# Optimization experiments

Measured on AMD Instinct MI355X. Metric: run time of the kernel, lower is better.

The kernel has to match this reference:

```python
import jax, jax.numpy as jnp
import numpy as np

# Static dims (match init_kwargs / input_specs)
N, F, C, H, W = 1, 60, 31, 64, 64
DIM = 60          # embed dim == F
WS = 8            # window_size
NH = 6            # num_heads
HD = DIM // NH    # head dim = 10
SHIFT = WS // 2   # shift for odd blocks
NWIN_TOK = WS * WS
MLP_HID = 4 * DIM
EPS = 1e-5


def _rel_pos_index(ws):
    # standard Swin relative position index, computed once in numpy
    coords = np.stack(np.meshgrid(np.arange(ws), np.arange(ws), indexing='ij'))  # (2, ws, ws)
    coords = coords.reshape(2, -1)                                                # (2, ws*ws)
    rel = coords[:, :, None] - coords[:, None, :]                                 # (2, n, n)
    rel = rel.transpose(1, 2, 0)
    rel[..., 0] += ws - 1
    rel[..., 1] += ws - 1
    rel[..., 0] *= 2 * ws - 1
    return rel.sum(-1)                                                            # (n, n)

RPI = jnp.asarray(_rel_pos_index(WS))  # (64, 64) int


def _attn_mask(h, w, ws, shift):
    # mask for shifted-window attention: -100 where tokens come from different regions
    img = np.zeros((h, w))
    cnt = 0
    for hs in (slice(0, -ws), slice(-ws, -shift), slice(-shift, None)):
        for wsl in (slice(0, -ws), slice(-ws, -shift), slice(-shift, None)):
            img[hs, wsl] = cnt
            cnt += 1
    m = img.reshape(h // ws, ws, w // ws, ws).transpose(0, 2, 1, 3).reshape(-1, ws * ws)  # (nW, n)
    diff = m[:, None, :] - m[:, :, None]
    return jnp.asarray(np.where(diff != 0, -100.0, 0.0).astype(np.float32))               # (nW, n, n)

ATTN_MASK = _attn_mask(H, W, WS, SHIFT)


def _ln(x, g, b):
    mu = jnp.mean(x, axis=-1, keepdims=True)
    var = jnp.mean(jnp.square(x - mu), axis=-1, keepdims=True)
    return (x - mu) * jax.lax.rsqrt(var + EPS) * g + b


def _swin_block(x, shift, g1, b1, qkv_w, qkv_b, rpb, proj_w, proj_b,
                g2, b2, fc1_w, fc1_b, fc2_w, fc2_b):
    # x: (B, L=H*W, DIM)
    B = x.shape[0]
    shortcut = x
    h = _ln(x, g1, b1).reshape(B, H, W, DIM)
    if shift > 0:
        h = jnp.roll(h, (-shift, -shift), axis=(1, 2))
    # window partition -> (B*nW, n, DIM)
    win = h.reshape(B, H // WS, WS, W // WS, WS, DIM).transpose(0, 1, 3, 2, 4, 5)
    win = win.reshape(-1, NWIN_TOK, DIM)
    Bw = win.shape[0]
    # qkv projection (torch Linear: y = x @ W.T + b)
    qkv = win @ qkv_w.T + qkv_b                                   # (Bw, n, 3*DIM)
    qkv = qkv.reshape(Bw, NWIN_TOK, 3, NH, HD).transpose(2, 0, 3, 1, 4)
    q, k, v = qkv[0], qkv[1], qkv[2]                              # (Bw, NH, n, HD)
    scale = HD ** -0.5
    attn = jnp.einsum('bhnd,bhmd->bhnm', q * scale, k)            # (Bw, NH, n, n)
    bias = rpb[RPI.reshape(-1)].reshape(NWIN_TOK, NWIN_TOK, NH).transpose(2, 0, 1)
    attn = attn + bias[None]
    if shift > 0:
        nW = ATTN_MASK.shape[0]
        attn = attn.reshape(-1, nW, NH, NWIN_TOK, NWIN_TOK) + ATTN_MASK[None, :, None]
        attn = attn.reshape(-1, NH, NWIN_TOK, NWIN_TOK)
    attn = jax.nn.softmax(attn, axis=-1)
    out = jnp.einsum('bhnm,bhmd->bhnd', attn, v).transpose(0, 2, 1, 3).reshape(Bw, NWIN_TOK, DIM)
    out = out @ proj_w.T + proj_b
    # window reverse -> (B, H, W, DIM)
    out = out.reshape(B, H // WS, W // WS, WS, WS, DIM).transpose(0, 1, 3, 2, 4, 5)
    out = out.reshape(B, H, W, DIM)
    if shift > 0:
        out = jnp.roll(out, (shift, shift), axis=(1, 2))
    x = shortcut + out.reshape(B, H * W, DIM)
    # MLP with exact GELU (torch nn.GELU default)
    h2 = _ln(x, g2, b2)
    h2 = jax.nn.gelu(h2 @ fc1_w.T + fc1_b, approximate=False) @ fc2_w.T + fc2_b
    return x + h2


def setup_inputs() -> dict:
    key = jax.random.key(0)
    ks = jax.random.split(key, 16)
    s = 0.02
    inp = {
        'x': jax.random.normal(ks[0], (N, F, C, H, W), jnp.float32),
        'norm1_g': jnp.ones((2, DIM), jnp.float32),
        'norm1_b': jnp.zeros((2, DIM), jnp.float32),
        'qkv_w': jax.random.normal(ks[1], (2, 3 * DIM, DIM), jnp.float32) * s,
        'qkv_b': jnp.zeros((2, 3 * DIM), jnp.float32),
        'rpb': jax.random.normal(ks[2], (2, (2 * WS - 1) ** 2, NH), jnp.float32) * s,
        'proj_w': jax.random.normal(ks[3], (2, DIM, DIM), jnp.float32) * s,
        'proj_b': jnp.zeros((2, DIM), jnp.float32),
        'norm2_g': jnp.ones((2, DIM), jnp.float32),
        'norm2_b': jnp.zeros((2, DIM), jnp.float32),
        'fc1_w': jax.random.normal(ks[4], (2, MLP_HID, DIM), jnp.float32) * s,
        'fc1_b': jnp.zeros((2, MLP_HID), jnp.float32),
        'fc2_w': jax.random.normal(ks[5], (2, DIM, MLP_HID), jnp.float32) * s,
        'fc2_b': jnp.zeros((2, DIM), jnp.float32),
    }
    return inp


def reference(x, norm1_g, norm1_b, qkv_w, qkv_b, rpb, proj_w, proj_b,
              norm2_g, norm2_b, fc1_w, fc1_b, fc2_w, fc2_b):
    # (N, F, C, H, W) -> (N*C, F, H, W) -> patch embed (flatten) -> (B, L, DIM)
    out = jnp.transpose(x, (0, 2, 1, 3, 4)).reshape(N * C, F, H, W)
    out = out.reshape(N * C, F, H * W).transpose(0, 2, 1)  # (B, L, DIM)
    for i in range(2):
        shift = 0 if i % 2 == 0 else SHIFT
        out = _swin_block(out, shift,
                          norm1_g[i], norm1_b[i], qkv_w[i], qkv_b[i], rpb[i],
                          proj_w[i], proj_b[i], norm2_g[i], norm2_b[i],
                          fc1_w[i], fc1_b[i], fc2_w[i], fc2_b[i])
    # patch unembed -> (B, F, H, W) -> (N, C, F, H, W) -> transpose(1,2)
    out = out.transpose(0, 2, 1).reshape(N * C, F, H, W)
    out = out.reshape(N, C, F, H, W)
    return jnp.transpose(out, (0, 2, 1, 3, 4))
```

## Files before the change

kernel.cpp:

```cpp
#include <hip/hip_runtime.h>
#include <hip/hip_bf16.h>
#include <math.h>


#define NB 31
#define NTOK 4096
#define DIM 60
#define NTOT (NB*NTOK)
#define QK_SCALE 0.31622776601683794f
#define LOG2E 1.4426950408889634f
#define QK_SCALE_L2E 0.45622000587446957f

typedef __attribute__((ext_vector_type(8))) short bf16x8;
typedef __attribute__((ext_vector_type(4))) float f32x4;

__device__ __forceinline__ short f2b(float f){
    return __builtin_bit_cast(short, __float2bfloat16(f));
}
__device__ __forceinline__ float b2f(unsigned short u){
    union{unsigned u;float f;}v; v.u=((unsigned)u)<<16; return v.f;
}
__device__ __forceinline__ unsigned pk2(float a,float b){
    return (unsigned)(unsigned short)f2b(a) | ((unsigned)(unsigned short)f2b(b)<<16);
}
#define MFMA16(a,b,c) __builtin_amdgcn_mfma_f32_16x16x32_bf16(a,b,c,0,0,0)
#define EXP2RAW(x) __builtin_amdgcn_exp2f(x)

#define PK_QKV  0
#define PK_PROJ 13824
#define PK_W1   18432
#define PK_W2   35712
#define PK_STRIDE 52608

__global__ __launch_bounds__(256) void pack_w(
    const float* __restrict__ qkv_w, const float* __restrict__ proj_w,
    const float* __restrict__ fc1_w, const float* __restrict__ fc2_w,
    const float* __restrict__ rpb, short* __restrict__ pk, float* __restrict__ btab)
{
    const int L = blockIdx.x;
    short* o = pk + (size_t)L * PK_STRIDE;
    const float* qw = qkv_w + L * 10800;
    const float* pw = proj_w + L * 3600;
    const float* w1 = fc1_w + L * 14400;
    const float* w2 = fc2_w + L * 14400;
    const float* rp = rpb + L * 1350;
    const int t0 = blockIdx.y * 256 + threadIdx.x;
    const int STP = 256 * gridDim.y;

    for (int i = t0; i < 192 * 72; i += STP) {
        int row = i / 72, k = i - row * 72;
        int p = row / 96, rg = row - p * 96;
        short v = 0;
        if (rg < 90 && k < 60) {
            int which = rg / 30, idx = rg - which * 30;
            int h = p * 3 + idx / 10, e = idx - (idx / 10) * 10;
            float wv = qw[(which * 60 + h * 10 + e) * 60 + k];
            if (which == 0) wv *= QK_SCALE_L2E;
            v = f2b(wv);
        }
        o[PK_QKV + i] = v;
    }
    for (int i = t0; i < 64 * 72; i += STP) {
        int n = i / 72, k = i - n * 72;
        o[PK_PROJ + i] = (n < 60 && k < 60) ? f2b(pw[n * 60 + k]) : (short)0;
    }
    for (int i = t0; i < 240 * 72; i += STP) {
        int n = i / 72, k = i - n * 72;
        o[PK_W1 + i] = (k < 60) ? f2b(w1[n * 60 + k]) : (short)0;
    }
    for (int i = t0; i < 64 * 264; i += STP) {
        int n = i / 264, k = i - n * 264;
        o[PK_W2 + i] = (n < 60 && k < 240) ? f2b(w2[n * 240 + k]) : (short)0;
    }
    const int NTAB = (L == 0) ? 24576 : 4 * 24576;
    float* bo = btab + (size_t)L * 4 * 24576;
    for (int i = t0; i < NTAB; i += STP) {
        int c = i / 24576, rem = i - c * 24576;
        int h = rem >> 12, rem2 = rem & 4095;
        int ii = rem2 >> 6, j = rem2 & 63;
        int iy = ii >> 3, ix = ii & 7, jy = j >> 3, jx = j & 7;
        float v = rp[((iy - jy + 7) * 15 + (ix - jx + 7)) * 6 + h];
        int riy = (c & 2) ? (iy < 4 ? 1 : 2) : 0;
        int rix = (c & 1) ? (ix < 4 ? 1 : 2) : 0;
        int rjy = (c & 2) ? (jy < 4 ? 1 : 2) : 0;
        int rjx = (c & 1) ? (jx < 4 ? 1 : 2) : 0;
        if (riy != rjy || rix != rjx) v -= 100.f;
        bo[i] = v * LOG2E;
    }
}

template<int L>
__global__ __launch_bounds__(256, 5) void swin_layer(
    const void* __restrict__ xin_v, void* __restrict__ xout_v,
    const float* __restrict__ g1, const float* __restrict__ b1,
    const float* __restrict__ g2, const float* __restrict__ b2,
    const short* __restrict__ pk, const float* __restrict__ btab,
    const float* __restrict__ qkv_b, const float* __restrict__ proj_b,
    const float* __restrict__ fc1_b, const float* __restrict__ fc2_b)
{
    __shared__ __attribute__((aligned(16))) short R1[64 * 72];
    __shared__ __attribute__((aligned(16))) short R2[8832];

    const f32x4 Z4 = {0.f, 0.f, 0.f, 0.f};
    const bf16x8 Z8 = {0, 0, 0, 0, 0, 0, 0, 0};

    const int tid = threadIdx.x;
    const int blk = ((blockIdx.x & 7) * 248) + (blockIdx.x >> 3);
    const int b = blk >> 6, w = blk & 63, wy = w >> 3, wx = w & 7;
    const int shift = L ? 4 : 0;
    const int cls = L ? (((wy == 7) ? 2 : 0) + ((wx == 7) ? 1 : 0)) : 0;

    const float* xf = (const float*)xin_v;
    const unsigned short* xb = (const unsigned short*)xin_v;

    for (int i = tid; i < 64 * 18; i += 256) {
        int row = i / 18, t = i - row * 18, bc = t / 3, k = t - bc * 3;
        *(int*)&R2[row * 104 + bc * 16 + 10 + 2 * k] = 0;
    }

    const int tk = tid >> 2, l4 = tid & 3;
    const int tok = (((wy * 8 + (tk >> 3) + shift) & 63) << 6)
                  + ((wx * 8 + (tk & 7) + shift) & 63);
    unsigned xpk[8];
    if (L == 0) {
        float xr[15]; float s = 0.f, s2 = 0.f;
#pragma unroll
        for (int dd = 0; dd < 15; ++dd) {
            float v = xf[(size_t)(l4 * 15 + dd) * NTOT + b * NTOK + tok];
            xr[dd] = v; s += v; s2 += v * v;
        }
        s  += __shfl_xor(s, 1);  s  += __shfl_xor(s, 2);
        s2 += __shfl_xor(s2, 1); s2 += __shfl_xor(s2, 2);
        const float mu = s * (1.f / 60.f);
        const float rs = rsqrtf(s2 * (1.f / 60.f) - mu * mu + 1e-5f);
#pragma unroll
        for (int dd = 0; dd < 15; ++dd) {
            int d = l4 * 15 + dd;
            R1[tk * 72 + d] = f2b((xr[dd] - mu) * rs * g1[d] + b1[d]);
        }
#pragma unroll
        for (int u = 0; u < 3; ++u) R1[tk * 72 + 60 + l4 * 3 + u] = 0;
#pragma unroll
        for (int u = 0; u < 7; ++u) xpk[u] = pk2(xr[2 * u], xr[2 * u + 1]);
        xpk[7] = pk2(xr[14], 0.f);
    } else {
        float xr[16]; float s = 0.f, s2 = 0.f;
        const int nd = (l4 == 3) ? 6 : 8, c0 = l4 * 16;
        const unsigned* rp_ = (const unsigned*)(xb + ((size_t)b * NTOK + tok) * DIM) + l4 * 8;
#pragma unroll
        for (int j = 0; j < 8; ++j) {
            if (j < nd) {
                unsigned u = rp_[j];
                xpk[j] = u;
                float v0 = b2f((unsigned short)(u & 0xffff));
                float v1 = b2f((unsigned short)(u >> 16));
                xr[2 * j] = v0; xr[2 * j + 1] = v1;
                s += v0 + v1; s2 += v0 * v0 + v1 * v1;
            }
        }
        s  += __shfl_xor(s, 1);  s  += __shfl_xor(s, 2);
        s2 += __shfl_xor(s2, 1); s2 += __shfl_xor(s2, 2);
        const float mu = s * (1.f / 60.f);
        const float rs = rsqrtf(s2 * (1.f / 60.f) - mu * mu + 1e-5f);
#pragma unroll
        for (int j = 0; j < 8; ++j) {
            if (j < nd) {
                int d = c0 + 2 * j;
                float n0 = (xr[2 * j] - mu) * rs * g1[d] + b1[d];
                float n1 = (xr[2 * j + 1] - mu) * rs * g1[d + 1] + b1[d + 1];
                *(unsigned*)&R1[tk * 72 + d] = pk2(n0, n1);
            }
        }
        if (l4 == 3) {
#pragma unroll
            for (int u = 0; u < 3; ++u) *(unsigned*)&R1[tk * 72 + 60 + 2 * u] = 0;
        }
    }

    const int lane = tid & 63, r16 = lane & 15, g = lane >> 4;
    const int m0 = (tid >> 6) << 4;

    bf16x8 a0 = *(const bf16x8*)&R1[(m0 + r16) * 72 + g * 8];
    bf16x8 a1 = *(const bf16x8*)&R1[(m0 + r16) * 72 + 32 + g * 8];
    const float* btc = btab + (size_t)cls * 24576 + (m0 + r16) * 64;

    for (int p = 0; p < 2; ++p) {
#pragma unroll
        for (int nt = 0; nt < 6; ++nt) {
            const short* wr = pk + PK_QKV + (size_t)(p * 96 + nt * 16 + r16) * 72;
            bf16x8 w0 = *(const bf16x8*)(wr + g * 8);
            bf16x8 w1v = *(const bf16x8*)(wr + 32 + g * 8);
            int c = nt * 16 + r16;
            int which = 0, hl = 0, e = 0; float bias = 0.f;
            if (c < 90) {
                which = c / 30; int idx = c - which * 30;
                hl = idx / 10; e = idx - hl * 10;
                bias = qkv_b[which * 60 + (p * 3 + hl) * 10 + e];
                if (which == 0) bias *= QK_SCALE_L2E;
            }
            f32x4 acc = {bias, bias, bias, bias};
            acc = MFMA16(a0, w0, acc);
            acc = MFMA16(a1, w1v, acc);
            if (c < 90) {
                if (which == 0) {
#pragma unroll
                    for (int r = 0; r < 4; ++r)
                        R2[(m0 + g * 4 + r) * 104 + hl * 16 + e] = f2b(acc[r]);
                } else if (which == 1) {
#pragma unroll
                    for (int r = 0; r < 4; ++r)
                        R2[(m0 + g * 4 + r) * 104 + 48 + hl * 16 + e] = f2b(acc[r]);
                } else {
#pragma unroll
                    for (int r = 0; r < 2; ++r)
                        *(unsigned*)&R2[6656 + (hl * 10 + e) * 72 + m0 + g * 4 + 2 * r] =
                            pk2(acc[2 * r], acc[2 * r + 1]);
                }
            }
        }
        __syncthreads();

#pragma unroll
        for (int hl = 0; hl < 3; ++hl) {
            const int h = p * 3 + hl;
            bf16x8 qa = Z8;
            if (g < 2) qa = *(const bf16x8*)&R2[(m0 + r16) * 104 + hl * 16 + g * 8];
            const float* bh = btc + h * 4096;
            f32x4 sv[4];
#pragma unroll
            for (int nt = 0; nt < 4; ++nt) {
                bf16x8 kb = Z8;
                if (g < 2) kb = *(const bf16x8*)&R2[(nt * 16 + r16) * 104 + 48 + hl * 16 + g * 8];
                sv[nt] = MFMA16(kb, qa, *(const f32x4*)&bh[nt * 16 + g * 4]);
            }
            float sum = 0.f;
#pragma unroll
            for (int nt = 0; nt < 4; ++nt)
#pragma unroll
                for (int r = 0; r < 4; ++r) {
                    float e = EXP2RAW(sv[nt][r]);
                    sv[nt][r] = e; sum += e;
                }
            sum += __shfl_xor(sum, 16);
            sum += __shfl_xor(sum, 32);
            const float inv = 1.f / sum;

            unsigned qd00 = pk2(sv[0][0], sv[0][1]), qd01 = pk2(sv[0][2], sv[0][3]);
            unsigned qd10 = pk2(sv[1][0], sv[1][1]), qd11 = pk2(sv[1][2], sv[1][3]);
            unsigned qd20 = pk2(sv[2][0], sv[2][1]), qd21 = pk2(sv[2][2], sv[2][3]);
            unsigned qd30 = pk2(sv[3][0], sv[3][1]), qd31 = pk2(sv[3][2], sv[3][3]);
            const int sA = (r16 + ((g & 1) << 5)) << 2;
            const int sB = sA + 64;
            const bool hi = (g >> 1) & 1;
            union { unsigned u[4]; bf16x8 v; } pb0, pb1;
            {
                unsigned x0 = __builtin_amdgcn_ds_bpermute(sA, (int)qd00);
                unsigned y0 = __builtin_amdgcn_ds_bpermute(sA, (int)qd10);
                pb0.u[0] = hi ? y0 : x0;
                unsigned x1 = __builtin_amdgcn_ds_bpermute(sA, (int)qd01);
                unsigned y1 = __builtin_amdgcn_ds_bpermute(sA, (int)qd11);
                pb0.u[1] = hi ? y1 : x1;
                unsigned x2 = __builtin_amdgcn_ds_bpermute(sB, (int)qd00);
                unsigned y2 = __builtin_amdgcn_ds_bpermute(sB, (int)qd10);
                pb0.u[2] = hi ? y2 : x2;
                unsigned x3 = __builtin_amdgcn_ds_bpermute(sB, (int)qd01);
                unsigned y3 = __builtin_amdgcn_ds_bpermute(sB, (int)qd11);
                pb0.u[3] = hi ? y3 : x3;
                unsigned u0 = __builtin_amdgcn_ds_bpermute(sA, (int)qd20);
                unsigned v0 = __builtin_amdgcn_ds_bpermute(sA, (int)qd30);
                pb1.u[0] = hi ? v0 : u0;
                unsigned u1 = __builtin_amdgcn_ds_bpermute(sA, (int)qd21);
                unsigned v1 = __builtin_amdgcn_ds_bpermute(sA, (int)qd31);
                pb1.u[1] = hi ? v1 : u1;
                unsigned u2 = __builtin_amdgcn_ds_bpermute(sB, (int)qd20);
                unsigned v2 = __builtin_amdgcn_ds_bpermute(sB, (int)qd30);
                pb1.u[2] = hi ? v2 : u2;
                unsigned u3 = __builtin_amdgcn_ds_bpermute(sB, (int)qd21);
                unsigned v3 = __builtin_amdgcn_ds_bpermute(sB, (int)qd31);
                pb1.u[3] = hi ? v3 : u3;
            }
            bf16x8 va0 = Z8, va1 = Z8;
            if (r16 < 10) {
                va0 = *(const bf16x8*)&R2[6656 + (hl * 10 + r16) * 72 + g * 8];
                va1 = *(const bf16x8*)&R2[6656 + (hl * 10 + r16) * 72 + 32 + g * 8];
            }
            f32x4 o = MFMA16(va0, pb0.v, Z4);
            o = MFMA16(va1, pb1.v, o);
            if (g < 2) {
                *(unsigned*)&R1[(m0 + r16) * 72 + h * 10 + g * 4]     = pk2(o[0] * inv, o[1] * inv);
                *(unsigned*)&R1[(m0 + r16) * 72 + h * 10 + g * 4 + 2] = pk2(o[2] * inv, o[3] * inv);
            } else if (g == 2) {
                *(unsigned*)&R1[(m0 + r16) * 72 + h * 10 + 8] = pk2(o[0] * inv, o[1] * inv);
            }
        }
        __syncthreads();
    }

    {
        bf16x8 oa0 = *(const bf16x8*)&R1[(m0 + r16) * 72 + g * 8];
        bf16x8 oa1 = *(const bf16x8*)&R1[(m0 + r16) * 72 + 32 + g * 8];
#pragma unroll
        for (int nt = 0; nt < 4; ++nt) {
            const short* wr = pk + PK_PROJ + (size_t)(nt * 16 + r16) * 72;
            bf16x8 w0 = *(const bf16x8*)(wr + g * 8);
            bf16x8 w1v = *(const bf16x8*)(wr + 32 + g * 8);
            int d = nt * 16 + r16;
            float pb_ = (d < 60) ? proj_b[d] : 0.f;
            f32x4 acc = {pb_, pb_, pb_, pb_};
            acc = MFMA16(oa0, w0, acc);
            acc = MFMA16(oa1, w1v, acc);
            if (d < 60) {
#pragma unroll
                for (int r = 0; r < 4; ++r)
                    R1[(m0 + g * 4 + r) * 72 + d] = f2b(acc[r]);
            }
        }
    }

    if (L == 0) {
        float yv[15]; float s = 0.f, s2 = 0.f;
#pragma unroll
        for (int dd = 0; dd < 15; ++dd) {
            int d = l4 * 15 + dd;
            float xv = b2f((unsigned short)((dd & 1) ? (xpk[dd >> 1] >> 16)
                                                    : (xpk[dd >> 1] & 0xffff)));
            float y = xv + b2f((unsigned short)R1[tk * 72 + d]);
            yv[dd] = y; s += y; s2 += y * y;
        }
        s  += __shfl_xor(s, 1);  s  += __shfl_xor(s, 2);
        s2 += __shfl_xor(s2, 1); s2 += __shfl_xor(s2, 2);
        const float mu = s * (1.f / 60.f);
        const float rs = rsqrtf(s2 * (1.f / 60.f) - mu * mu + 1e-5f);
#pragma unroll
        for (int dd = 0; dd < 15; ++dd) {
            int d = l4 * 15 + dd;
            R1[tk * 72 + d] = f2b(yv[dd]);
            R2[tk * 136 + d] = f2b((yv[dd] - mu) * rs * g2[d] + b2[d]);
        }
#pragma unroll
        for (int u = 0; u < 3; ++u) R2[tk * 136 + 60 + l4 * 3 + u] = 0;
    } else {
        float yv[16]; float s = 0.f, s2 = 0.f;
        const int nd = (l4 == 3) ? 6 : 8, c0 = l4 * 16;
#pragma unroll
        for (int j = 0; j < 8; ++j) {
            if (j < nd) {
                int d = c0 + 2 * j;
                float y0 = b2f((unsigned short)(xpk[j] & 0xffff))
                         + b2f((unsigned short)R1[tk * 72 + d]);
                float y1 = b2f((unsigned short)(xpk[j] >> 16))
                         + b2f((unsigned short)R1[tk * 72 + d + 1]);
                yv[2 * j] = y0; yv[2 * j + 1] = y1;
                s += y0 + y1; s2 += y0 * y0 + y1 * y1;
            }
        }
        s  += __shfl_xor(s, 1);  s  += __shfl_xor(s, 2);
        s2 += __shfl_xor(s2, 1); s2 += __shfl_xor(s2, 2);
        const float mu = s * (1.f / 60.f);
        const float rs = rsqrtf(s2 * (1.f / 60.f) - mu * mu + 1e-5f);
#pragma unroll
        for (int j = 0; j < 8; ++j) {
            if (j < nd) {
                int d = c0 + 2 * j;
                *(unsigned*)&R1[tk * 72 + d] = pk2(yv[2 * j], yv[2 * j + 1]);
                float n0 = (yv[2 * j] - mu) * rs * g2[d] + b2[d];
                float n1 = (yv[2 * j + 1] - mu) * rs * g2[d + 1] + b2[d + 1];
                *(unsigned*)&R2[tk * 136 + d] = pk2(n0, n1);
            }
        }
        if (l4 == 3) {
#pragma unroll
            for (int u = 0; u < 3; ++u) *(unsigned*)&R2[tk * 136 + 60 + 2 * u] = 0;
        }
    }

    bf16x8 la0 = *(const bf16x8*)&R2[(m0 + r16) * 136 + g * 8];
    bf16x8 la1 = *(const bf16x8*)&R2[(m0 + r16) * 136 + 32 + g * 8];

    f32x4 acc2[4];
#pragma unroll
    for (int nt = 0; nt < 4; ++nt) {
        int d = nt * 16 + r16;
        float fb = (d < 60) ? fc2_b[d] : 0.f;
        acc2[nt] = (f32x4){fb, fb, fb, fb};
    }

#pragma unroll
    for (int nt = 0; nt < 8; ++nt) {
        const short* wr = pk + PK_W1 + (size_t)(nt * 16 + r16) * 72;
        bf16x8 w0 = *(const bf16x8*)(wr + g * 8);
        bf16x8 w1v = *(const bf16x8*)(wr + 32 + g * 8);
        int c = nt * 16 + r16;
        float fb = fc1_b[c];
        f32x4 acc = {fb, fb, fb, fb};
        acc = MFMA16(la0, w0, acc);
        acc = MFMA16(la1, w1v, acc);
#pragma unroll
        for (int r = 0; r < 4; ++r) {
            float u = acc[r];
            float zz = 2.302208235f * u + 0.10294353f * (u * u * u);
            float ge = u * __builtin_amdgcn_rcpf(1.f + EXP2RAW(-zz));
            R2[(m0 + g * 4 + r) * 136 + c] = f2b(ge);
        }
    }
#pragma unroll
    for (int kk = 0; kk < 4; ++kk) {
        bf16x8 ha = *(const bf16x8*)&R2[(m0 + r16) * 136 + kk * 32 + g * 8];
#pragma unroll
        for (int nt = 0; nt < 4; ++nt) {
            const short* wr = pk + PK_W2 + (size_t)(nt * 16 + r16) * 264 + kk * 32 + g * 8;
            acc2[nt] = MFMA16(ha, *(const bf16x8*)wr, acc2[nt]);
        }
    }
    *(int*)&R2[(m0 + r16) * 136 + 112 + g * 4]     = 0;
    *(int*)&R2[(m0 + r16) * 136 + 112 + g * 4 + 2] = 0;
#pragma unroll
    for (int nt = 0; nt < 7; ++nt) {
        const short* wr = pk + PK_W1 + (size_t)(128 + nt * 16 + r16) * 72;
        bf16x8 w0 = *(const bf16x8*)(wr + g * 8);
        bf16x8 w1v = *(const bf16x8*)(wr + 32 + g * 8);
        int c = nt * 16 + r16;
        float fb = fc1_b[128 + c];
        f32x4 acc = {fb, fb, fb, fb};
        acc = MFMA16(la0, w0, acc);
        acc = MFMA16(la1, w1v, acc);
#pragma unroll
        for (int r = 0; r < 4; ++r) {
            float u = acc[r];
            float zz = 2.302208235f * u + 0.10294353f * (u * u * u);
            float ge = u * __builtin_amdgcn_rcpf(1.f + EXP2RAW(-zz));
            R2[(m0 + g * 4 + r) * 136 + c] = f2b(ge);
        }
    }
#pragma unroll
    for (int kk = 0; kk < 4; ++kk) {
        bf16x8 ha = *(const bf16x8*)&R2[(m0 + r16) * 136 + kk * 32 + g * 8];
#pragma unroll
        for (int nt = 0; nt < 4; ++nt) {
            const short* wr = pk + PK_W2 + (size_t)(nt * 16 + r16) * 264 + 128 + kk * 32 + g * 8;
            acc2[nt] = MFMA16(ha, *(const bf16x8*)wr, acc2[nt]);
        }
    }

#pragma unroll
    for (int nt = 0; nt < 4; ++nt) {
        int d = nt * 16 + r16;
        if (d < 60) {
#pragma unroll
            for (int r = 0; r < 4; ++r) {
                float yv = b2f((unsigned short)R1[(m0 + g * 4 + r) * 72 + d]);
                float v = yv + acc2[nt][r];
                if (L == 0) R2[(m0 + g * 4 + r) * 136 + d] = f2b(v);
                else        ((float*)R2)[(m0 + g * 4 + r) * 68 + d] = v;
            }
        }
    }
    __syncthreads();

    if (L == 0) {
        unsigned* ob = (unsigned*)xout_v;
        const size_t gbase = (size_t)b * NTOK * 30;
        for (int i = tid; i < 1920; i += 256) {
            int r = i / 30, c = i - r * 30;
            int gt = ((wy * 8 + (r >> 3)) << 6) + wx * 8 + (r & 7);
            ob[gbase + (size_t)gt * 30 + c] = *(unsigned*)&R2[r * 136 + 2 * c];
        }
    } else {
        float* of = (float*)xout_v;
        for (int i = tid; i < 3840; i += 256) {
            int d = i >> 6, t = i & 63;
            int gt = (((wy * 8 + (t >> 3) + 4) & 63) << 6) + ((wx * 8 + (t & 7) + 4) & 63);
            of[(size_t)d * NTOT + b * NTOK + gt] = ((const float*)R2)[t * 68 + d];
        }
    }
}

extern "C" void kernel_launch(void* const* d_in, const int* in_sizes, int n_in,
                              void* d_out, int out_size, void* d_ws, size_t ws_size,
                              hipStream_t stream)
{
    const float* x       = (const float*)d_in[0];
    const float* norm1_g = (const float*)d_in[1];
    const float* norm1_b = (const float*)d_in[2];
    const float* qkv_w   = (const float*)d_in[3];
    const float* qkv_b   = (const float*)d_in[4];
    const float* rpb     = (const float*)d_in[5];
    const float* proj_w  = (const float*)d_in[6];
    const float* proj_b  = (const float*)d_in[7];
    const float* norm2_g = (const float*)d_in[8];
    const float* norm2_b = (const float*)d_in[9];
    const float* fc1_w   = (const float*)d_in[10];
    const float* fc1_b   = (const float*)d_in[11];
    const float* fc2_w   = (const float*)d_in[12];
    const float* fc2_b   = (const float*)d_in[13];

    unsigned short* bufA = (unsigned short*)d_ws;
    short* pk  = (short*)((char*)d_ws + (size_t)NTOT * DIM * 2);
    float* btab = (float*)((char*)pk + 2 * PK_STRIDE * 2);

    dim3 block(256);
    pack_w<<<dim3(2, 64), block, 0, stream>>>(qkv_w, proj_w, fc1_w, fc2_w, rpb, pk, btab);

    dim3 grid(NB * 64);
    swin_layer<0><<<grid, block, 0, stream>>>(
        (const void*)x, (void*)bufA,
        norm1_g, norm1_b, norm2_g, norm2_b, pk, btab,
        qkv_b, proj_b, fc1_b, fc2_b);
    swin_layer<1><<<grid, block, 0, stream>>>(
        (const void*)bufA, d_out,
        norm1_g + 60, norm1_b + 60, norm2_g + 60, norm2_b + 60,
        pk + PK_STRIDE, btab + 4 * 24576,
        qkv_b + 180, proj_b + 60, fc1_b + 240, fc2_b + 60);

    (void)in_sizes; (void)n_in; (void)out_size; (void)ws_size;
}
```

Measured before the change: 163.0 us.

## Split each fused Swin layer into separate attention and MLP kernels

Each fused per-window layer kernel becomes two launches. An attention kernel writes the residual sum in bf16, un-shifted to a global buffer, and an MLP kernel reads tokens linearly and applies LN2, fc1, GELU, fc2 and the residual. The d_out buffer holds the intermediate between layers. This may lower register and LDS pressure per kernel and simplify the MLP indexing, at the cost of an extra global round trip of activations and two more launches.

```diff
diff --git a/kernel.cpp b/kernel.cpp
--- a/kernel.cpp
+++ b/kernel.cpp
@@ -90,16 +90,14 @@
 }
 
 template<int L>
-__global__ __launch_bounds__(256, 5) void swin_layer(
-    const void* __restrict__ xin_v, void* __restrict__ xout_v,
+__global__ __launch_bounds__(256, 5) void swin_attn(
+    const void* __restrict__ xin_v, unsigned short* __restrict__ yout,
     const float* __restrict__ g1, const float* __restrict__ b1,
-    const float* __restrict__ g2, const float* __restrict__ b2,
     const short* __restrict__ pk, const float* __restrict__ btab,
-    const float* __restrict__ qkv_b, const float* __restrict__ proj_b,
-    const float* __restrict__ fc1_b, const float* __restrict__ fc2_b)
+    const float* __restrict__ qkv_b, const float* __restrict__ proj_b)
 {
     __shared__ __attribute__((aligned(16))) short R1[64 * 72];
-    __shared__ __attribute__((aligned(16))) short R2[8832];
+    __shared__ __attribute__((aligned(16))) short R2[8816];
 
     const f32x4 Z4 = {0.f, 0.f, 0.f, 0.f};
     const bf16x8 Z8 = {0, 0, 0, 0, 0, 0, 0, 0};
@@ -318,29 +316,14 @@
     }
 
     if (L == 0) {
-        float yv[15]; float s = 0.f, s2 = 0.f;
 #pragma unroll
         for (int dd = 0; dd < 15; ++dd) {
             int d = l4 * 15 + dd;
             float xv = b2f((unsigned short)((dd & 1) ? (xpk[dd >> 1] >> 16)
                                                     : (xpk[dd >> 1] & 0xffff)));
-            float y = xv + b2f((unsigned short)R1[tk * 72 + d]);
-            yv[dd] = y; s += y; s2 += y * y;
-        }
-        s  += __shfl_xor(s, 1);  s  += __shfl_xor(s, 2);
-        s2 += __shfl_xor(s2, 1); s2 += __shfl_xor(s2, 2);
-        const float mu = s * (1.f / 60.f);
-        const float rs = rsqrtf(s2 * (1.f / 60.f) - mu * mu + 1e-5f);
-#pragma unroll
-        for (int dd = 0; dd < 15; ++dd) {
-            int d = l4 * 15 + dd;
-            R1[tk * 72 + d] = f2b(yv[dd]);
-            R2[tk * 136 + d] = f2b((yv[dd] - mu) * rs * g2[d] + b2[d]);
-        }
-#pragma unroll
-        for (int u = 0; u < 3; ++u) R2[tk * 136 + 60 + l4 * 3 + u] = 0;
+            R2[tk * 136 + d] = f2b(xv + b2f((unsigned short)R1[tk * 72 + d]));
+        }
     } else {
-        float yv[16]; float s = 0.f, s2 = 0.f;
         const int nd = (l4 == 3) ? 6 : 8, c0 = l4 * 16;
 #pragma unroll
         for (int j = 0; j < 8; ++j) {
@@ -350,8 +333,52 @@
                          + b2f((unsigned short)R1[tk * 72 + d]);
                 float y1 = b2f((unsigned short)(xpk[j] >> 16))
                          + b2f((unsigned short)R1[tk * 72 + d + 1]);
-                yv[2 * j] = y0; yv[2 * j + 1] = y1;
-                s += y0 + y1; s2 += y0 * y0 + y1 * y1;
+                *(unsigned*)&R2[tk * 136 + d] = pk2(y0, y1);
+            }
+        }
+    }
+    __syncthreads();
+
+    {
+        unsigned* ob = (unsigned*)yout;
+        const size_t gbase = (size_t)b * NTOK * 30;
+        for (int i = tid; i < 1920; i += 256) {
+            int r = i / 30, c = i - r * 30;
+            int gt = (((wy * 8 + (r >> 3) + shift) & 63) << 6)
+                   + ((wx * 8 + (r & 7) + shift) & 63);
+            ob[gbase + (size_t)gt * 30 + c] = *(unsigned*)&R2[r * 136 + 2 * c];
+        }
+    }
+}
+
+template<int OUTF>
+__global__ __launch_bounds__(256, 5) void swin_mlp(
+    const unsigned short* __restrict__ yin, void* __restrict__ xout_v,
+    const float* __restrict__ g2, const float* __restrict__ b2,
+    const short* __restrict__ pk,
+    const float* __restrict__ fc1_b, const float* __restrict__ fc2_b)
+{
+    __shared__ __attribute__((aligned(16))) short Ry[64 * 72];
+    __shared__ __attribute__((aligned(16))) short R2[8704];
+
+    const int tid = threadIdx.x;
+    const size_t t0 = (size_t)blockIdx.x * 64;
+    const int tk = tid >> 2, l4 = tid & 3;
+
+    {
+        float yr[16]; float s = 0.f, s2 = 0.f;
+        const int nd = (l4 == 3) ? 6 : 8, c0 = l4 * 16;
+        unsigned ypk[8];
+        const unsigned* rp_ = (const unsigned*)(yin + (t0 + tk) * DIM) + l4 * 8;
+#pragma unroll
+        for (int j = 0; j < 8; ++j) {
+            if (j < nd) {
+                unsigned u = rp_[j];
+                ypk[j] = u;
+                float v0 = b2f((unsigned short)(u & 0xffff));
+                float v1 = b2f((unsigned short)(u >> 16));
+                yr[2 * j] = v0; yr[2 * j + 1] = v1;
+                s += v0 + v1; s2 += v0 * v0 + v1 * v1;
             }
         }
         s  += __shfl_xor(s, 1);  s  += __shfl_xor(s, 2);
@@ -362,9 +389,9 @@
         for (int j = 0; j < 8; ++j) {
             if (j < nd) {
                 int d = c0 + 2 * j;
-                *(unsigned*)&R1[tk * 72 + d] = pk2(yv[2 * j], yv[2 * j + 1]);
-                float n0 = (yv[2 * j] - mu) * rs * g2[d] + b2[d];
-                float n1 = (yv[2 * j + 1] - mu) * rs * g2[d + 1] + b2[d + 1];
+                *(unsigned*)&Ry[tk * 72 + d] = ypk[j];
+                float n0 = (yr[2 * j] - mu) * rs * g2[d] + b2[d];
+                float n1 = (yr[2 * j + 1] - mu) * rs * g2[d + 1] + b2[d + 1];
                 *(unsigned*)&R2[tk * 136 + d] = pk2(n0, n1);
             }
         }
@@ -373,6 +400,9 @@
             for (int u = 0; u < 3; ++u) *(unsigned*)&R2[tk * 136 + 60 + 2 * u] = 0;
         }
     }
+
+    const int lane = tid & 63, r16 = lane & 15, g = lane >> 4;
+    const int m0 = (tid >> 6) << 4;
 
     bf16x8 la0 = *(const bf16x8*)&R2[(m0 + r16) * 136 + g * 8];
     bf16x8 la1 = *(const bf16x8*)&R2[(m0 + r16) * 136 + 32 + g * 8];
@@ -384,6 +414,9 @@
         float fb = (d < 60) ? fc2_b[d] : 0.f;
         acc2[nt] = (f32x4){fb, fb, fb, fb};
     }
+
+    const f32x4 Z4 = {0.f, 0.f, 0.f, 0.f};
+    (void)Z4;
 
 #pragma unroll
     for (int nt = 0; nt < 8; ++nt) {
@@ -448,29 +481,27 @@
         if (d < 60) {
 #pragma unroll
             for (int r = 0; r < 4; ++r) {
-                float yv = b2f((unsigned short)R1[(m0 + g * 4 + r) * 72 + d]);
+                float yv = b2f((unsigned short)Ry[(m0 + g * 4 + r) * 72 + d]);
                 float v = yv + acc2[nt][r];
-                if (L == 0) R2[(m0 + g * 4 + r) * 136 + d] = f2b(v);
-                else        ((float*)R2)[(m0 + g * 4 + r) * 68 + d] = v;
+                if (OUTF == 0) R2[(m0 + g * 4 + r) * 136 + d] = f2b(v);
+                else           ((float*)R2)[(m0 + g * 4 + r) * 68 + d] = v;
             }
         }
     }
     __syncthreads();
 
-    if (L == 0) {
+    if (OUTF == 0) {
         unsigned* ob = (unsigned*)xout_v;
-        const size_t gbase = (size_t)b * NTOK * 30;
+        const size_t gbase = t0 * 30;
         for (int i = tid; i < 1920; i += 256) {
             int r = i / 30, c = i - r * 30;
-            int gt = ((wy * 8 + (r >> 3)) << 6) + wx * 8 + (r & 7);
-            ob[gbase + (size_t)gt * 30 + c] = *(unsigned*)&R2[r * 136 + 2 * c];
+            ob[gbase + (size_t)r * 30 + c] = *(unsigned*)&R2[r * 136 + 2 * c];
         }
     } else {
         float* of = (float*)xout_v;
         for (int i = tid; i < 3840; i += 256) {
-            int d = i >> 6, t = i & 63;
-            int gt = (((wy * 8 + (t >> 3) + 4) & 63) << 6) + ((wx * 8 + (t & 7) + 4) & 63);
-            of[(size_t)d * NTOT + b * NTOK + gt] = ((const float*)R2)[t * 68 + d];
+            int d = i >> 6, tt = i & 63;
+            of[(size_t)d * NTOT + t0 + tt] = ((const float*)R2)[tt * 68 + d];
         }
     }
 }
@@ -497,20 +528,22 @@
     unsigned short* bufA = (unsigned short*)d_ws;
     short* pk  = (short*)((char*)d_ws + (size_t)NTOT * DIM * 2);
     float* btab = (float*)((char*)pk + 2 * PK_STRIDE * 2);
+    unsigned short* xB = (unsigned short*)d_out;
 
     dim3 block(256);
     pack_w<<<dim3(2, 64), block, 0, stream>>>(qkv_w, proj_w, fc1_w, fc2_w, rpb, pk, btab);
 
     dim3 grid(NB * 64);
-    swin_layer<0><<<grid, block, 0, stream>>>(
-        (const void*)x, (void*)bufA,
-        norm1_g, norm1_b, norm2_g, norm2_b, pk, btab,
-        qkv_b, proj_b, fc1_b, fc2_b);
-    swin_layer<1><<<grid, block, 0, stream>>>(
-        (const void*)bufA, d_out,
-        norm1_g + 60, norm1_b + 60, norm2_g + 60, norm2_b + 60,
-        pk + PK_STRIDE, btab + 4 * 24576,
-        qkv_b + 180, proj_b + 60, fc1_b + 240, fc2_b + 60);
+    swin_attn<0><<<grid, block, 0, stream>>>(
+        (const void*)x, bufA, norm1_g, norm1_b, pk, btab, qkv_b, proj_b);
+    swin_mlp<0><<<grid, block, 0, stream>>>(
+        bufA, (void*)xB, norm2_g, norm2_b, pk, fc1_b, fc2_b);
+    swin_attn<1><<<grid, block, 0, stream>>>(
+        (const void*)xB, bufA, norm1_g + 60, norm1_b + 60,
+        pk + PK_STRIDE, btab + 4 * 24576, qkv_b + 180, proj_b + 60);
+    swin_mlp<1><<<grid, block, 0, stream>>>(
+        bufA, d_out, norm2_g + 60, norm2_b + 60,
+        pk + PK_STRIDE, fc1_b + 240, fc2_b + 60);
 
     (void)in_sizes; (void)n_in; (void)out_size; (void)ws_size;
 }
```

After: 177.0 us. +8.6%, slower.
